# Kernel optimization log

Hardware: AMD Instinct MI355X
Metric: run time of the kernel (lower is better)

## Reference

```python
import jax, jax.numpy as jnp
import numpy as np

DIM = 768
NUM_HEADS = 12
HEAD_DIM = DIM // NUM_HEADS
SCALE = HEAD_DIM ** -0.5


def setup_inputs() -> dict:
    key = jax.random.key(0)
    k_x, k_qkv, k_pw, k_pb = jax.random.split(key, 4)
    x = jax.random.normal(k_x, (1, 4096, DIM), dtype=jnp.float32)
    # nn.Linear weights stored as [out, in]; apply as x @ W.T
    w_qkv = jax.random.normal(k_qkv, (3 * DIM, DIM), dtype=jnp.float32) * (DIM ** -0.5)
    w_proj = jax.random.normal(k_pw, (DIM, DIM), dtype=jnp.float32) * (DIM ** -0.5)
    b_proj = jax.random.normal(k_pb, (DIM,), dtype=jnp.float32) * 0.01
    return {"x": x, "w_qkv": w_qkv, "w_proj": w_proj, "b_proj": b_proj}


def reference(x, w_qkv, w_proj, b_proj):
    b, s, d = x.shape
    qkv = jnp.einsum('bsd,ed->bse', x, w_qkv)            # [B,S,3D]
    qkv = qkv.reshape(b, s, 3, NUM_HEADS, HEAD_DIM)
    qkv = jnp.transpose(qkv, (2, 0, 3, 1, 4))            # [3,B,H,S,hd]
    q, k, v = qkv[0], qkv[1], qkv[2]
    scores = jnp.einsum('bhqe,bhke->bhqk', q, k) * SCALE  # [B,H,S,S]
    probs = jax.nn.softmax(scores, axis=-1)
    attended = jnp.einsum('bhqk,bhke->bhqe', probs, v)    # [B,H,S,hd]
    attended = jnp.transpose(attended, (0, 2, 1, 3)).reshape(b, s, d)
    return jnp.einsum('bsd,ed->bse', attended, w_proj) + b_proj
```

## Files before the change

kernel.cpp:

```cpp
#include <hip/hip_runtime.h>
#include <hip/hip_bf16.h>

using short8 = __attribute__((ext_vector_type(8))) short;
using s16x4  = __attribute__((ext_vector_type(4))) short;
using f32x2  = __attribute__((ext_vector_type(2))) float;
using f32x4  = __attribute__((ext_vector_type(4))) float;
using f32x16 = __attribute__((ext_vector_type(16))) float;
using v2i    = __attribute__((ext_vector_type(2))) int;

#define DIM   768
#define D3    2304
#define SEQL  4096
#define NHEAD 12
#define NSPLIT 2

#if defined(__has_builtin)
#  if __has_builtin(__builtin_amdgcn_permlane32_swap)
#    define HAVE_PLSWAP 1
#  endif
#endif

static __device__ __forceinline__ short f2bs(float f) {
  union { __hip_bfloat16 h; short s; } u;
  u.h = __float2bfloat16(f);
  return u.s;
}

static __device__ __forceinline__ float bf2f(short s) {
  union { unsigned u; float f; } x;
  x.u = ((unsigned)(unsigned short)s) << 16;
  return x.f;
}

static __device__ __forceinline__ int cvtpk(float lo, float hi) {
  int r;
  asm("v_cvt_pk_bf16_f32 %0, %1, %2" : "=v"(r) : "v"(lo), "v"(hi));
  return r;
}

static __device__ __forceinline__ f32x2 pkadd(f32x2 a, f32x2 b) {
  f32x2 r;
  asm("v_pk_add_f32 %0, %1, %2" : "=v"(r) : "v"(a), "v"(b));
  return r;
}

static __device__ __forceinline__ float ex2(float x) {
  float r;
  asm("v_exp_f32 %0, %1" : "=v"(r) : "v"(x));
  return r;
}

static __device__ __forceinline__ void gl_lds16(const void* g, void* lds) {
  __builtin_amdgcn_global_load_lds((const __attribute__((address_space(1))) void*)g,
                                   (__attribute__((address_space(3))) void*)lds, 16, 0, 0);
}

__global__ __launch_bounds__(256) void cvt3_kernel(const float* __restrict__ x,
                                                   const float* __restrict__ wq,
                                                   const float* __restrict__ wp,
                                                   short* __restrict__ xb,
                                                   short* __restrict__ wqb,
                                                   short* __restrict__ wpb) {
  int b = blockIdx.x;
  const float* src; short* dst; int base; float sc = 1.0f;
  if (b < 3072)      { src = x;  dst = xb;  base = b * 1024; }
  else if (b < 4800) { src = wq; dst = wqb; base = (b - 3072) * 1024;
                       if (base < DIM * DIM) sc = 0.125f * 1.4426950408889634f; }
  else               { src = wp; dst = wpb; base = (b - 4800) * 1024; }
  int i = base + threadIdx.x * 4;
  f32x4 v = *(const f32x4*)(src + i);
  s16x4 o;
  #pragma unroll
  for (int j = 0; j < 4; ++j) o[j] = f2bs(v[j] * sc);
  *(s16x4*)(dst + i) = o;
}

template <bool BF16OUT>
__global__ __launch_bounds__(256) void gemm_bt(const short* __restrict__ A,
                                               const short* __restrict__ B,
                                               short* __restrict__ Cb,
                                               float* __restrict__ Cf,
                                               const float* __restrict__ bias,
                                               int M, int N, int K) {
  __shared__ short As[128 * 64];
  __shared__ short Bs[128 * 64];
  const int tid = threadIdx.x;
  const int l  = tid & 63;
  const int w  = tid >> 6;
  const int g  = l >> 4, lc = l & 15;
  const int wr = w >> 1, wc = w & 1;
  const int m0 = blockIdx.y * 128, n0 = blockIdx.x * 128;
  const int trow = tid >> 3;
  const int tcol = (tid & 7) * 8;
  const int sswz = 8 * (trow & 7);
  const int rswz = 8 * (lc & 7);

  f32x4 acc[4][4];
  #pragma unroll
  for (int a = 0; a < 4; ++a)
    #pragma unroll
    for (int b = 0; b < 4; ++b) acc[a][b] = (f32x4){0.f, 0.f, 0.f, 0.f};

  for (int k0 = 0; k0 < K; k0 += 64) {
    __syncthreads();
    #pragma unroll
    for (int i = 0; i < 4; ++i) {
      int row = i * 32 + trow;
      gl_lds16(A + (size_t)(m0 + row) * K + k0 + (tcol ^ sswz), As + row * 64 + tcol);
      gl_lds16(B + (size_t)(n0 + row) * K + k0 + (tcol ^ sswz), Bs + row * 64 + tcol);
    }
    __syncthreads();
    #pragma unroll
    for (int kk = 0; kk < 2; ++kk) {
      short8 af[4], bf[4];
      #pragma unroll
      for (int mt = 0; mt < 4; ++mt)
        af[mt] = *(const short8*)(As + (wr * 64 + mt * 16 + lc) * 64 + ((kk * 32 + g * 8) ^ rswz));
      #pragma unroll
      for (int nt = 0; nt < 4; ++nt)
        bf[nt] = *(const short8*)(Bs + (wc * 64 + nt * 16 + lc) * 64 + ((kk * 32 + g * 8) ^ rswz));
      #pragma unroll
      for (int mt = 0; mt < 4; ++mt)
        #pragma unroll
        for (int nt = 0; nt < 4; ++nt)
          acc[mt][nt] = __builtin_amdgcn_mfma_f32_16x16x32_bf16(af[mt], bf[nt], acc[mt][nt], 0, 0, 0);
    }
  }

  #pragma unroll
  for (int mt = 0; mt < 4; ++mt)
    #pragma unroll
    for (int nt = 0; nt < 4; ++nt)
      #pragma unroll
      for (int r = 0; r < 4; ++r) {
        int row = m0 + wr * 64 + mt * 16 + g * 4 + r;
        int col = n0 + wc * 64 + nt * 16 + lc;
        float v = acc[mt][nt][r];
        if (BF16OUT) Cb[(size_t)row * N + col] = f2bs(v);
        else         Cf[(size_t)row * N + col] = v + bias[col];
      }
}

template <bool BF16OUT>
__global__ __launch_bounds__(256) void gemm_bt64(const short* __restrict__ A,
                                                 const short* __restrict__ B,
                                                 short* __restrict__ Cb,
                                                 float* __restrict__ Cf,
                                                 const float* __restrict__ bias,
                                                 int M, int N, int K) {
  __shared__ short As[64 * 64];
  __shared__ short Bs[64 * 64];
  const int tid = threadIdx.x;
  const int l  = tid & 63;
  const int w  = tid >> 6;
  const int g  = l >> 4, lc = l & 15;
  const int wr = w >> 1, wc = w & 1;
  const int m0 = blockIdx.y * 64, n0 = blockIdx.x * 64;
  const int rswz = 8 * (lc & 7);

  f32x4 acc[2][2];
  #pragma unroll
  for (int a = 0; a < 2; ++a)
    #pragma unroll
    for (int b = 0; b < 2; ++b) acc[a][b] = (f32x4){0.f, 0.f, 0.f, 0.f};

  for (int k0 = 0; k0 < K; k0 += 64) {
    __syncthreads();
    #pragma unroll
    for (int i = 0; i < 2; ++i) {
      int seg = i * 256 + tid;
      int row = seg >> 3, c = (seg & 7) * 8;
      int swz = 8 * (row & 7);
      gl_lds16(A + (size_t)(m0 + row) * K + k0 + (c ^ swz), As + seg * 8);
      gl_lds16(B + (size_t)(n0 + row) * K + k0 + (c ^ swz), Bs + seg * 8);
    }
    __syncthreads();
    #pragma unroll
    for (int kk = 0; kk < 2; ++kk) {
      short8 af[2], bf[2];
      #pragma unroll
      for (int mt = 0; mt < 2; ++mt)
        af[mt] = *(const short8*)(As + (wr * 32 + mt * 16 + lc) * 64 + ((kk * 32 + g * 8) ^ rswz));
      #pragma unroll
      for (int nt = 0; nt < 2; ++nt)
        bf[nt] = *(const short8*)(Bs + (wc * 32 + nt * 16 + lc) * 64 + ((kk * 32 + g * 8) ^ rswz));
      #pragma unroll
      for (int mt = 0; mt < 2; ++mt)
        #pragma unroll
        for (int nt = 0; nt < 2; ++nt)
          acc[mt][nt] = __builtin_amdgcn_mfma_f32_16x16x32_bf16(af[mt], bf[nt], acc[mt][nt], 0, 0, 0);
    }
  }

  #pragma unroll
  for (int mt = 0; mt < 2; ++mt)
    #pragma unroll
    for (int nt = 0; nt < 2; ++nt)
      #pragma unroll
      for (int r = 0; r < 4; ++r) {
        int row = m0 + wr * 32 + mt * 16 + g * 4 + r;
        int col = n0 + wc * 32 + nt * 16 + lc;
        float v = acc[mt][nt][r];
        if (BF16OUT) Cb[(size_t)row * N + col] = f2bs(v);
        else         Cf[(size_t)row * N + col] = v + bias[col];
      }
}

__global__ __launch_bounds__(256) void transpose_v(const short* __restrict__ qkv,
                                                   short* __restrict__ vtg) {
  __shared__ short T[64][72];
  const int jt = blockIdx.x, hd = blockIdx.y, tid = threadIdx.x;
  #pragma unroll
  for (int i = 0; i < 2; ++i) {
    int idx = i * 256 + tid;
    int r = idx >> 3, c = idx & 7;
    *(short8*)&T[r][8 * c] =
        *(const short8*)(qkv + (size_t)(jt * 64 + r) * D3 + 1536 + hd * 64 + 8 * c);
  }
  __syncthreads();
  #pragma unroll
  for (int i = 0; i < 2; ++i) {
    int idx = i * 256 + tid;
    int d = idx >> 3, jc = idx & 7;
    short8 v;
    #pragma unroll
    for (int e = 0; e < 8; ++e) v[e] = T[8 * jc + e][d];
    *(short8*)(vtg + ((size_t)hd * 64 + d) * 4096 + jt * 64 + 8 * jc) = v;
  }
}

__global__ __launch_bounds__(256) void attn_kernel(const short* __restrict__ qkv,
                                                   const short* __restrict__ vtg,
                                                   short* __restrict__ O0,
                                                   short* __restrict__ O1,
                                                   float* __restrict__ Lp,
                                                   int tpb) {
  __shared__ short Ks[3][64 * 64];
  __shared__ short Vt[3][64 * 64];

  const int lin = blockIdx.x;
  const int swz = (lin & 7) * 96 + (lin >> 3);
  const int qt   = swz & 31;
  const int head = (swz >> 5) % NHEAD;
  const int z    = swz / (32 * NHEAD);

  const int tid = threadIdx.x;
  const int l = tid & 63, w = tid >> 6;
  const int h = l >> 5;
  const int q5 = l & 31;
  const int hoff = head * 64;
  const int qbase = qt * 128 + w * 32;
  const int t0 = z * tpb, tend = t0 + tpb;

  short8 qf[4];
  {
    const short* qrow = qkv + (size_t)(qbase + q5) * D3 + hoff;
    #pragma unroll
    for (int ks = 0; ks < 4; ++ks) qf[ks] = *(const short8*)(qrow + ks * 16 + h * 8);
  }

  f32x16 o[2];
  #pragma unroll
  for (int nt = 0; nt < 2; ++nt)
    #pragma unroll
    for (int r = 0; r < 16; ++r) o[nt][r] = 0.f;
  float l_run = 0.f;
  const f32x16 zacc = {};

  const int swzK = 8 * (q5 & 7);

  const int srow = tid >> 3, scol = (tid & 7) * 8;
  const int sswz = 8 * (srow & 7);
  const short* kptr = qkv + (size_t)(t0 * 64 + srow) * D3 + hoff + 768 + (scol ^ sswz);
  const short* vptr = vtg + ((size_t)hoff + srow) * 4096 + t0 * 64 + (scol ^ sswz);

  #define STAGE(BUF)                                                             \
    {                                                                            \
      gl_lds16(kptr,             &Ks[BUF][tid * 8]);                             \
      gl_lds16(kptr + 32 * D3,   &Ks[BUF][(tid + 256) * 8]);                     \
      gl_lds16(vptr,             &Vt[BUF][tid * 8]);                             \
      gl_lds16(vptr + 32 * 4096, &Vt[BUF][(tid + 256) * 8]);                     \
      kptr += 64 * D3;                                                           \
      vptr += 64;                                                                \
    }

  STAGE(0);
  STAGE(1);

  int cur = 0, sb = 2;
  for (int tt = t0; tt < tend; ++tt) {
    if (tt + 1 < tend) asm volatile("s_waitcnt vmcnt(4)" ::: "memory");
    else               asm volatile("s_waitcnt vmcnt(0)" ::: "memory");
    __builtin_amdgcn_s_barrier();
    if (tt + 2 < tend) STAGE(sb);

    f32x16 p[2];
    __builtin_amdgcn_s_setprio(1);
    #pragma unroll
    for (int ks = 0; ks < 4; ++ks) {
      #pragma unroll
      for (int mt = 0; mt < 2; ++mt) {
        short8 kf = *(const short8*)(&Ks[cur][(mt * 32 + q5) * 64
                                              + ((ks * 16 + h * 8) ^ swzK)]);
        p[mt] = __builtin_amdgcn_mfma_f32_32x32x16_bf16(kf, qf[ks],
                                                        ks == 0 ? zacc : p[mt], 0, 0, 0);
      }
    }
    __builtin_amdgcn_s_setprio(0);

    f32x2 s2 = {0.f, 0.f};
    #pragma unroll
    for (int mt = 0; mt < 2; ++mt)
      #pragma unroll
      for (int i = 0; i < 8; ++i) {
        float pe0 = ex2(p[mt][2 * i]);
        float pe1 = ex2(p[mt][2 * i + 1]);
        p[mt][2 * i] = pe0;
        p[mt][2 * i + 1] = pe1;
        s2 = pkadd(s2, (f32x2){pe0, pe1});
      }
    l_run += s2[0] + s2[1];

    int D[16];
    #pragma unroll
    for (int mt = 0; mt < 2; ++mt)
      #pragma unroll
      for (int c = 0; c < 4; ++c) {
        D[mt * 8 + c * 2 + 0] = cvtpk(p[mt][4 * c + 0], p[mt][4 * c + 1]);
        D[mt * 8 + c * 2 + 1] = cvtpk(p[mt][4 * c + 2], p[mt][4 * c + 3]);
      }

    __builtin_amdgcn_s_setprio(1);
    #pragma unroll
    for (int ks = 0; ks < 4; ++ks) {
      union { int i[4]; short8 s; } pa;
#ifdef HAVE_PLSWAP
      v2i r02 = __builtin_amdgcn_permlane32_swap(D[4 * ks + 0], D[4 * ks + 2], false, false);
      v2i r13 = __builtin_amdgcn_permlane32_swap(D[4 * ks + 1], D[4 * ks + 3], false, false);
      pa.i[0] = r02[0];
      pa.i[1] = r13[0];
      pa.i[2] = r02[1];
      pa.i[3] = r13[1];
#else
      const bool hh = (h != 0);
      const int a0 = D[4 * ks + 0], a1 = D[4 * ks + 1];
      const int b0 = D[4 * ks + 2], b1 = D[4 * ks + 3];
      int snd0 = hh ? a0 : b0, snd1 = hh ? a1 : b1;
      int r0 = __shfl_xor(snd0, 32), r1 = __shfl_xor(snd1, 32);
      pa.i[0] = hh ? r0 : a0;
      pa.i[1] = hh ? r1 : a1;
      pa.i[2] = hh ? b0 : r0;
      pa.i[3] = hh ? b1 : r1;
#endif
      #pragma unroll
      for (int nt = 0; nt < 2; ++nt) {
        short8 vf = *(const short8*)(&Vt[cur][(nt * 32 + q5) * 64
                                              + ((ks * 16 + h * 8) ^ swzK)]);
        o[nt] = __builtin_amdgcn_mfma_f32_32x32x16_bf16(pa.s, vf, o[nt], 0, 0, 0);
      }
    }
    __builtin_amdgcn_s_setprio(0);

    cur = (cur == 2) ? 0 : cur + 1;
    sb  = (sb == 2) ? 0 : sb + 1;
  }

  float l_tot = l_run + __shfl_xor(l_run, 32);
  if (h == 0) Lp[(size_t)z * SEQL * NHEAD + (qbase + q5) * NHEAD + head] = l_tot;
  short* Ob = (z == 0) ? O0 : O1;
  #pragma unroll
  for (int nt = 0; nt < 2; ++nt)
    #pragma unroll
    for (int pp = 0; pp < 4; ++pp)
      #pragma unroll
      for (int r = 0; r < 4; ++r) {
        int q = qbase + r + 8 * pp + 4 * h;
        int d = hoff + nt * 32 + q5;
        Ob[(size_t)q * DIM + d] = f2bs(o[nt][4 * pp + r]);
      }
}

__global__ __launch_bounds__(256) void combine_kernel(short* __restrict__ O0,
                                                      const short* __restrict__ O1,
                                                      const float* __restrict__ Lp) {
  int idx = blockIdx.x * 256 + threadIdx.x;
  int e0 = idx * 8;
  if (e0 >= SEQL * DIM) return;
  int q = e0 / DIM, col = e0 % DIM, head = col >> 6;
  float lv = Lp[q * NHEAD + head] + Lp[SEQL * NHEAD + q * NHEAD + head];
  float inv = 1.0f / lv;
  short8 a = *(const short8*)(O0 + e0);
  short8 b = *(const short8*)(O1 + e0);
  short8 r;
  #pragma unroll
  for (int j = 0; j < 8; ++j) r[j] = f2bs((bf2f(a[j]) + bf2f(b[j])) * inv);
  *(short8*)(O0 + e0) = r;
}

extern "C" void kernel_launch(void* const* d_in, const int* in_sizes, int n_in,
                              void* d_out, int out_size, void* d_ws, size_t ws_size,
                              hipStream_t stream) {
  (void)in_sizes; (void)n_in; (void)out_size; (void)ws_size;
  const float* x      = (const float*)d_in[0];
  const float* w_qkv  = (const float*)d_in[1];
  const float* w_proj = (const float*)d_in[2];
  const float* b_proj = (const float*)d_in[3];
  float* out = (float*)d_out;

  short* xb   = (short*)d_ws;
  short* wqb  = xb  + (size_t)SEQL * DIM;
  short* wpb  = wqb + (size_t)D3 * DIM;
  short* qkvb = wpb + (size_t)DIM * DIM;
  short* attb = qkvb + (size_t)SEQL * D3;
  short* Opart1 = xb;
  float* Lpart  = (float*)wqb;
  short* vtg    = (short*)d_out;

  cvt3_kernel<<<5376, 256, 0, stream>>>(x, w_qkv, w_proj, xb, wqb, wpb);
  gemm_bt<true ><<<dim3(D3 / 128, SEQL / 128), 256, 0, stream>>>(xb, wqb, qkvb, nullptr, nullptr, SEQL, D3, DIM);
  transpose_v<<<dim3(SEQL / 64, NHEAD), 256, 0, stream>>>(qkvb, vtg);
  attn_kernel<<<dim3(32 * NHEAD * NSPLIT, 1, 1), 256, 0, stream>>>(qkvb, vtg, attb, Opart1, Lpart,
                                                                   (SEQL / 64) / NSPLIT);
  combine_kernel<<<SEQL * DIM / 8 / 256, 256, 0, stream>>>(attb, Opart1, Lpart);
  gemm_bt64<false><<<dim3(DIM / 64, SEQL / 64), 256, 0, stream>>>(attb, wpb, nullptr, out, b_proj, SEQL, DIM, DIM);
}
```

Baseline: 126.5 us.

## Write V transposed directly from QKV GEMM and compute row sums via MFMA

The QKV GEMM now has two block roles. One group computes Q and K into a narrower buffer. The other computes V^T directly as W_v·x^T into the transposed layout the attention kernel reads, so the separate transpose kernel and the V round trip through memory are gone. In the attention loop, the softmax denominator is no longer accumulated with scalar adds; an extra MFMA against a vector of ones sums it, moving VALU work onto the matrix unit at the cost of one more MFMA per k-step and 16 more accumulator registers.

```diff
diff --git a/kernel.cpp b/kernel.cpp
--- a/kernel.cpp
+++ b/kernel.cpp
@@ -3,13 +3,13 @@
 
 using short8 = __attribute__((ext_vector_type(8))) short;
 using s16x4  = __attribute__((ext_vector_type(4))) short;
-using f32x2  = __attribute__((ext_vector_type(2))) float;
 using f32x4  = __attribute__((ext_vector_type(4))) float;
 using f32x16 = __attribute__((ext_vector_type(16))) float;
 using v2i    = __attribute__((ext_vector_type(2))) int;
 
 #define DIM   768
 #define D3    2304
+#define QKS   1536
 #define SEQL  4096
 #define NHEAD 12
 #define NSPLIT 2
@@ -35,12 +35,6 @@
 static __device__ __forceinline__ int cvtpk(float lo, float hi) {
   int r;
   asm("v_cvt_pk_bf16_f32 %0, %1, %2" : "=v"(r) : "v"(lo), "v"(hi));
-  return r;
-}
-
-static __device__ __forceinline__ f32x2 pkadd(f32x2 a, f32x2 b) {
-  f32x2 r;
-  asm("v_pk_add_f32 %0, %1, %2" : "=v"(r) : "v"(a), "v"(b));
   return r;
 }
 
@@ -75,21 +69,22 @@
   *(s16x4*)(dst + i) = o;
 }
 
-template <bool BF16OUT>
-__global__ __launch_bounds__(256) void gemm_bt(const short* __restrict__ A,
-                                               const short* __restrict__ B,
-                                               short* __restrict__ Cb,
-                                               float* __restrict__ Cf,
-                                               const float* __restrict__ bias,
-                                               int M, int N, int K) {
+__global__ __launch_bounds__(256) void gemm_qkv(const short* __restrict__ xb,
+                                                const short* __restrict__ wqb,
+                                                short* __restrict__ qkb,
+                                                short* __restrict__ vtg) {
   __shared__ short As[128 * 64];
   __shared__ short Bs[128 * 64];
+  const int bx = blockIdx.x, by = blockIdx.y;
+  const short *A, *B; short* C; int m0, n0, ldc;
+  if (bx < 12) { A = xb;                     B = wqb; C = qkb; m0 = by * 128; n0 = bx * 128;        ldc = QKS; }
+  else         { A = wqb + 1536 * DIM;       B = xb;  C = vtg; m0 = (bx - 12) * 128; n0 = by * 128; ldc = SEQL; }
+
   const int tid = threadIdx.x;
   const int l  = tid & 63;
   const int w  = tid >> 6;
   const int g  = l >> 4, lc = l & 15;
   const int wr = w >> 1, wc = w & 1;
-  const int m0 = blockIdx.y * 128, n0 = blockIdx.x * 128;
   const int trow = tid >> 3;
   const int tcol = (tid & 7) * 8;
   const int sswz = 8 * (trow & 7);
@@ -101,13 +96,13 @@
     #pragma unroll
     for (int b = 0; b < 4; ++b) acc[a][b] = (f32x4){0.f, 0.f, 0.f, 0.f};
 
-  for (int k0 = 0; k0 < K; k0 += 64) {
+  for (int k0 = 0; k0 < DIM; k0 += 64) {
     __syncthreads();
     #pragma unroll
     for (int i = 0; i < 4; ++i) {
       int row = i * 32 + trow;
-      gl_lds16(A + (size_t)(m0 + row) * K + k0 + (tcol ^ sswz), As + row * 64 + tcol);
-      gl_lds16(B + (size_t)(n0 + row) * K + k0 + (tcol ^ sswz), Bs + row * 64 + tcol);
+      gl_lds16(A + (size_t)(m0 + row) * DIM + k0 + (tcol ^ sswz), As + row * 64 + tcol);
+      gl_lds16(B + (size_t)(n0 + row) * DIM + k0 + (tcol ^ sswz), Bs + row * 64 + tcol);
     }
     __syncthreads();
     #pragma unroll
@@ -135,9 +130,7 @@
       for (int r = 0; r < 4; ++r) {
         int row = m0 + wr * 64 + mt * 16 + g * 4 + r;
         int col = n0 + wc * 64 + nt * 16 + lc;
-        float v = acc[mt][nt][r];
-        if (BF16OUT) Cb[(size_t)row * N + col] = f2bs(v);
-        else         Cf[(size_t)row * N + col] = v + bias[col];
+        C[(size_t)row * ldc + col] = f2bs(acc[mt][nt][r]);
       }
 }
 
@@ -206,30 +199,7 @@
       }
 }
 
-__global__ __launch_bounds__(256) void transpose_v(const short* __restrict__ qkv,
-                                                   short* __restrict__ vtg) {
-  __shared__ short T[64][72];
-  const int jt = blockIdx.x, hd = blockIdx.y, tid = threadIdx.x;
-  #pragma unroll
-  for (int i = 0; i < 2; ++i) {
-    int idx = i * 256 + tid;
-    int r = idx >> 3, c = idx & 7;
-    *(short8*)&T[r][8 * c] =
-        *(const short8*)(qkv + (size_t)(jt * 64 + r) * D3 + 1536 + hd * 64 + 8 * c);
-  }
-  __syncthreads();
-  #pragma unroll
-  for (int i = 0; i < 2; ++i) {
-    int idx = i * 256 + tid;
-    int d = idx >> 3, jc = idx & 7;
-    short8 v;
-    #pragma unroll
-    for (int e = 0; e < 8; ++e) v[e] = T[8 * jc + e][d];
-    *(short8*)(vtg + ((size_t)hd * 64 + d) * 4096 + jt * 64 + 8 * jc) = v;
-  }
-}
-
-__global__ __launch_bounds__(256) void attn_kernel(const short* __restrict__ qkv,
+__global__ __launch_bounds__(256) void attn_kernel(const short* __restrict__ qkb,
                                                    const short* __restrict__ vtg,
                                                    short* __restrict__ O0,
                                                    short* __restrict__ O1,
@@ -254,33 +224,36 @@
 
   short8 qf[4];
   {
-    const short* qrow = qkv + (size_t)(qbase + q5) * D3 + hoff;
+    const short* qrow = qkb + (size_t)(qbase + q5) * QKS + hoff;
     #pragma unroll
     for (int ks = 0; ks < 4; ++ks) qf[ks] = *(const short8*)(qrow + ks * 16 + h * 8);
   }
 
-  f32x16 o[2];
+  f32x16 o[2], o_l;
   #pragma unroll
   for (int nt = 0; nt < 2; ++nt)
     #pragma unroll
     for (int r = 0; r < 16; ++r) o[nt][r] = 0.f;
-  float l_run = 0.f;
+  #pragma unroll
+  for (int r = 0; r < 16; ++r) o_l[r] = 0.f;
   const f32x16 zacc = {};
+  const short8 ones8 = {(short)0x3F80, (short)0x3F80, (short)0x3F80, (short)0x3F80,
+                        (short)0x3F80, (short)0x3F80, (short)0x3F80, (short)0x3F80};
 
   const int swzK = 8 * (q5 & 7);
 
   const int srow = tid >> 3, scol = (tid & 7) * 8;
   const int sswz = 8 * (srow & 7);
-  const short* kptr = qkv + (size_t)(t0 * 64 + srow) * D3 + hoff + 768 + (scol ^ sswz);
+  const short* kptr = qkb + (size_t)(t0 * 64 + srow) * QKS + hoff + 768 + (scol ^ sswz);
   const short* vptr = vtg + ((size_t)hoff + srow) * 4096 + t0 * 64 + (scol ^ sswz);
 
   #define STAGE(BUF)                                                             \
     {                                                                            \
       gl_lds16(kptr,             &Ks[BUF][tid * 8]);                             \
-      gl_lds16(kptr + 32 * D3,   &Ks[BUF][(tid + 256) * 8]);                     \
+      gl_lds16(kptr + 32 * QKS,  &Ks[BUF][(tid + 256) * 8]);                     \
       gl_lds16(vptr,             &Vt[BUF][tid * 8]);                             \
       gl_lds16(vptr + 32 * 4096, &Vt[BUF][(tid + 256) * 8]);                     \
-      kptr += 64 * D3;                                                           \
+      kptr += 64 * QKS;                                                          \
       vptr += 64;                                                                \
     }
 
@@ -308,18 +281,10 @@
     }
     __builtin_amdgcn_s_setprio(0);
 
-    f32x2 s2 = {0.f, 0.f};
     #pragma unroll
     for (int mt = 0; mt < 2; ++mt)
       #pragma unroll
-      for (int i = 0; i < 8; ++i) {
-        float pe0 = ex2(p[mt][2 * i]);
-        float pe1 = ex2(p[mt][2 * i + 1]);
-        p[mt][2 * i] = pe0;
-        p[mt][2 * i + 1] = pe1;
-        s2 = pkadd(s2, (f32x2){pe0, pe1});
-      }
-    l_run += s2[0] + s2[1];
+      for (int i = 0; i < 16; ++i) p[mt][i] = ex2(p[mt][i]);
 
     int D[16];
     #pragma unroll
@@ -352,6 +317,7 @@
       pa.i[2] = hh ? b0 : r0;
       pa.i[3] = hh ? b1 : r1;
 #endif
+      o_l = __builtin_amdgcn_mfma_f32_32x32x16_bf16(pa.s, ones8, o_l, 0, 0, 0);
       #pragma unroll
       for (int nt = 0; nt < 2; ++nt) {
         short8 vf = *(const short8*)(&Vt[cur][(nt * 32 + q5) * 64
@@ -365,8 +331,13 @@
     sb  = (sb == 2) ? 0 : sb + 1;
   }
 
-  float l_tot = l_run + __shfl_xor(l_run, 32);
-  if (h == 0) Lp[(size_t)z * SEQL * NHEAD + (qbase + q5) * NHEAD + head] = l_tot;
+  if (q5 == 0) {
+    #pragma unroll
+    for (int pp = 0; pp < 4; ++pp)
+      #pragma unroll
+      for (int r = 0; r < 4; ++r)
+        Lp[(size_t)z * SEQL * NHEAD + (qbase + r + 8 * pp + 4 * h) * NHEAD + head] = o_l[4 * pp + r];
+  }
   short* Ob = (z == 0) ? O0 : O1;
   #pragma unroll
   for (int nt = 0; nt < 2; ++nt)
@@ -410,16 +381,15 @@
   short* xb   = (short*)d_ws;
   short* wqb  = xb  + (size_t)SEQL * DIM;
   short* wpb  = wqb + (size_t)D3 * DIM;
-  short* qkvb = wpb + (size_t)DIM * DIM;
-  short* attb = qkvb + (size_t)SEQL * D3;
+  short* qkb  = wpb + (size_t)DIM * DIM;
+  short* attb = qkb + (size_t)SEQL * QKS;
   short* Opart1 = xb;
   float* Lpart  = (float*)wqb;
   short* vtg    = (short*)d_out;
 
   cvt3_kernel<<<5376, 256, 0, stream>>>(x, w_qkv, w_proj, xb, wqb, wpb);
-  gemm_bt<true ><<<dim3(D3 / 128, SEQL / 128), 256, 0, stream>>>(xb, wqb, qkvb, nullptr, nullptr, SEQL, D3, DIM);
-  transpose_v<<<dim3(SEQL / 64, NHEAD), 256, 0, stream>>>(qkvb, vtg);
-  attn_kernel<<<dim3(32 * NHEAD * NSPLIT, 1, 1), 256, 0, stream>>>(qkvb, vtg, attb, Opart1, Lpart,
+  gemm_qkv<<<dim3(18, 32), 256, 0, stream>>>(xb, wqb, qkb, vtg);
+  attn_kernel<<<dim3(32 * NHEAD * NSPLIT, 1, 1), 256, 0, stream>>>(qkb, vtg, attb, Opart1, Lpart,
                                                                    (SEQL / 64) / NSPLIT);
   combine_kernel<<<SEQL * DIM / 8 / 256, 256, 0, stream>>>(attb, Opart1, Lpart);
   gemm_bt64<false><<<dim3(DIM / 64, SEQL / 64), 256, 0, stream>>>(attb, wpb, nullptr, out, b_proj, SEQL, DIM, DIM);
```

Result: slower. 130.0 us (+2.8%).
